# Kernel optimization log

Measured on AMD Instinct MI355X. Metric: run time of the kernel, lower is better.

## Reference

```python
import jax, jax.numpy as jnp
import numpy as np

B, T, IN, H = 1024, 200, 128, 128

def _linear_params(key, out_dim, in_dim):
    kw, kb = jax.random.split(key)
    bound = 1.0 / np.sqrt(in_dim)
    w = jax.random.uniform(kw, (out_dim, in_dim), jnp.float32, -bound, bound)
    b = jax.random.uniform(kb, (out_dim,), jnp.float32, -bound, bound)
    return w, b

def setup_inputs() -> dict:
    key = jax.random.key(0)
    ks = jax.random.split(key, 10)
    targets = jax.random.normal(ks[0], (B, T, IN), jnp.float32)
    history_states = jax.random.normal(ks[1], (B, T, H), jnp.float32)
    W_w, W_b = _linear_params(ks[2], H, IN)
    xu_w, xu_b = _linear_params(ks[3], H, H)
    hu_w, hu_b = _linear_params(ks[4], H, H)
    xr_w, xr_b = _linear_params(ks[5], H, H)
    hr_w, hr_b = _linear_params(ks[6], H, H)
    xg_w, xg_b = _linear_params(ks[7], H, H)
    hg_w, hg_b = _linear_params(ks[8], H, H)
    ln2_w, ln2_b = _linear_params(ks[9], H, IN + H)
    return dict(targets=targets, history_states=history_states,
                W_w=W_w, W_b=W_b, xu_w=xu_w, xu_b=xu_b, hu_w=hu_w, hu_b=hu_b,
                xr_w=xr_w, xr_b=xr_b, hr_w=hr_w, hr_b=hr_b,
                xg_w=xg_w, xg_b=xg_b, hg_w=hg_w, hg_b=hg_b,
                ln2_w=ln2_w, ln2_b=ln2_b)

def reference(targets, history_states, W_w, W_b, xu_w, xu_b, hu_w, hu_b,
              xr_w, xr_b, hr_w, hr_b, xg_w, xg_b, hg_w, hg_b, ln2_w, ln2_b):
    # attention weights: softmax over time of <W(targets), history>
    aw = jnp.einsum('bti,hi->bth', targets, W_w) + W_b            # [B,T,H]
    att = jax.nn.softmax(jnp.sum(aw * history_states, -1, keepdims=True), axis=1)  # [B,T,1]

    # precompute input-side projections as big GEMMs (same math as per-step Linear)
    xu = jnp.einsum('bth,oh->bto', history_states, xu_w) + xu_b   # [B,T,H]
    xr = jnp.einsum('bth,oh->bto', history_states, xr_w) + xr_b
    xg = jnp.einsum('bth,oh->bto', history_states, xg_w) + xg_b

    def step(h, xs):
        xu_t, xr_t, xg_t, a_t = xs                                 # [B,H],[B,H],[B,H],[B,1]
        u = jax.nn.sigmoid(xu_t + h @ hu_w.T + hu_b) * a_t
        r = jax.nn.sigmoid(xr_t + h @ hr_w.T + hr_b)
        g = jnp.tanh(xg_t + r * (h @ hg_w.T + hg_b))
        h = (1.0 - u) * h + u * g
        return h, None

    h0 = jnp.zeros((targets.shape[0], hu_w.shape[0]), targets.dtype)
    # scan over time: move T to leading axis
    xs = (jnp.swapaxes(xu, 0, 1), jnp.swapaxes(xr, 0, 1),
          jnp.swapaxes(xg, 0, 1), jnp.swapaxes(att, 0, 1))
    h, _ = jax.lax.scan(step, h0, xs)

    out = jnp.concatenate([h, targets[:, 0]], axis=-1) @ ln2_w.T + ln2_b
    return out
```

## Files before the change

kernel.cpp:

```cpp
#include <hip/hip_runtime.h>

#define B_ 1024
#define T_ 200
#define H_ 128

typedef __attribute__((ext_vector_type(8))) short short8;
typedef __attribute__((ext_vector_type(4))) float f32x4;

#define MFMA(a, b, c) __builtin_amdgcn_mfma_f32_16x16x32_bf16((a), (b), (c), 0, 0, 0)

static __device__ __forceinline__ short f2bf(float f) {
  unsigned u = __float_as_uint(f);
  u += 0x7fffu + ((u >> 16) & 1u);
  return (short)(u >> 16);
}
static __device__ __forceinline__ float bf2f(short s) {
  return __uint_as_float(((unsigned)(unsigned short)s) << 16);
}
static __device__ __forceinline__ unsigned pack2bf_rne(float a, float b) {
  unsigned ua = __float_as_uint(a);
  ua += 0x7fffu + ((ua >> 16) & 1u);
  unsigned ub = __float_as_uint(b);
  ub += 0x7fffu + ((ub >> 16) & 1u);
  return (ua >> 16) | (ub & 0xFFFF0000u);
}
static __device__ __forceinline__ unsigned pack2bf_trunc(float a, float b) {
  return (__float_as_uint(a) >> 16) | (__float_as_uint(b) & 0xFFFF0000u);
}
static __device__ __forceinline__ float rcp_f(float x) { return __builtin_amdgcn_rcpf(x); }
static __device__ __forceinline__ void ck_barrier() {
  asm volatile("s_waitcnt lgkmcnt(0)\n\ts_barrier" ::: "memory");
}

__global__ __launch_bounds__(512, 1) void proj_scores_kernel(
    const float* __restrict__ tgt, const float* __restrict__ hist,
    const float* __restrict__ Ww, const float* __restrict__ Wb,
    float* __restrict__ scores, short* __restrict__ histbf) {
  const int tc = blockIdx.x, bb = blockIdx.y;
  const int nt = (tc == 12) ? 8 : 16;
  const int t0 = tc * 16;
  const int tid = threadIdx.x;
  const int lane = tid & 63, w = tid >> 6;
  const int n = lane & 15, q = lane >> 4;

  __shared__ short tgt_hi[2][16 * 128];
  __shared__ short tgt_lo[2][16 * 128];
  __shared__ float hist_f[2][16 * 132];
  __shared__ float sp[16 * 8];

  short8 whi[4], wlo[4];
  f32x4 wb4;
  {
    const int o = w * 16 + n;
#pragma unroll
    for (int ks = 0; ks < 4; ++ks) {
      const float* p = Ww + o * H_ + ks * 32 + q * 8;
      short8 h, l;
#pragma unroll
      for (int j = 0; j < 8; ++j) {
        float f = p[j];
        short hv = f2bf(f);
        h[j] = hv;
        l[j] = f2bf(f - bf2f(hv));
      }
      whi[ks] = h;
      wlo[ks] = l;
    }
    wb4 = *(const f32x4*)(Wb + w * 16 + q * 4);
  }

  const int sm = tid >> 5, cs = tid & 31;
  const int g = cs >> 1, half = cs & 1;
  const int spos16 = sm * 128 + ((g ^ (sm & 7)) * 8) + half * 4;
  const int sposf = sm * 132 + cs * 4;
  const size_t rowbase = ((size_t)(bb * 16 + sm) * T_) * H_ + cs * 4;

  const int cu = tid;
  const int cks = cu >> 7, crem = cu & 127, cwl = crem >> 1, chalf = crem & 1;
  const int crow = cwl & 15, ckb = cks * 32 + (cwl >> 4) * 8 + chalf * 4;

  float4 hv = *(const float4*)(hist + rowbase + (size_t)t0 * H_);
  float4 tv = *(const float4*)(tgt + rowbase + (size_t)t0 * H_);
  {
    *(float4*)&hist_f[0][sposf] = hv;
    uint2 hi, lo;
    hi.x = pack2bf_rne(tv.x, tv.y);
    hi.y = pack2bf_rne(tv.z, tv.w);
    lo.x = pack2bf_rne(tv.x - bf2f((short)(hi.x)), tv.y - bf2f((short)(hi.x >> 16)));
    lo.y = pack2bf_rne(tv.z - bf2f((short)(hi.y)), tv.w - bf2f((short)(hi.y >> 16)));
    *(uint2*)&tgt_hi[0][spos16] = hi;
    *(uint2*)&tgt_lo[0][spos16] = lo;
  }
  ck_barrier();

  for (int tl = 0; tl < nt; ++tl) {
    const int cur = tl & 1, nxt = cur ^ 1;
    const bool have_next = (tl + 1 < nt);
    if (have_next) {
      hv = *(const float4*)(hist + rowbase + (size_t)(t0 + tl + 1) * H_);
      tv = *(const float4*)(tgt + rowbase + (size_t)(t0 + tl + 1) * H_);
    }
    f32x4 s1 = {0, 0, 0, 0}, s2 = {0, 0, 0, 0}, s3 = {0, 0, 0, 0};
#pragma unroll
    for (int ks = 0; ks < 4; ++ks) {
      const int fp = n * 128 + ((ks * 4 + q) ^ (n & 7)) * 8;
      short8 ahi = *(short8*)&tgt_hi[cur][fp];
      short8 alo = *(short8*)&tgt_lo[cur][fp];
      s1 = MFMA(whi[ks], ahi, s1);
      s2 = MFMA(wlo[ks], ahi, s2);
      s3 = MFMA(whi[ks], alo, s3);
    }
    {
      f32x4 hv4 = *(const f32x4*)&hist_f[cur][n * 132 + w * 16 + q * 4];
      float v = (s1[0] + s2[0] + s3[0] + wb4[0]) * hv4[0];
      v += (s1[1] + s2[1] + s3[1] + wb4[1]) * hv4[1];
      v += (s1[2] + s2[2] + s3[2] + wb4[2]) * hv4[2];
      v += (s1[3] + s2[3] + s3[3] + wb4[3]) * hv4[3];
      v += __shfl_xor(v, 16);
      v += __shfl_xor(v, 32);
      if (lane < 16) sp[n * 8 + w] = v;
    }
    if (histbf != nullptr) {
      const float* src = &hist_f[cur][crow * 132 + ckb];
      uint2 u;
      u.x = pack2bf_rne(src[0], src[1]);
      u.y = pack2bf_rne(src[2], src[3]);
      const size_t sb = (((size_t)(bb * T_ + t0 + tl) * 4) + cks) * 512 + cwl * 8 + chalf * 4;
      *(uint2*)(histbf + sb) = u;
    }
    if (have_next) {
      *(float4*)&hist_f[nxt][sposf] = hv;
      uint2 hi, lo;
      hi.x = pack2bf_rne(tv.x, tv.y);
      hi.y = pack2bf_rne(tv.z, tv.w);
      lo.x = pack2bf_rne(tv.x - bf2f((short)(hi.x)), tv.y - bf2f((short)(hi.x >> 16)));
      lo.y = pack2bf_rne(tv.z - bf2f((short)(hi.y)), tv.w - bf2f((short)(hi.y >> 16)));
      *(uint2*)&tgt_hi[nxt][spos16] = hi;
      *(uint2*)&tgt_lo[nxt][spos16] = lo;
    }
    ck_barrier();
    if (tid < 16) {
      float s = 0.0f;
#pragma unroll
      for (int ww = 0; ww < 8; ++ww) s += sp[tid * 8 + ww];
      scores[(size_t)(bb * 16 + tid) * T_ + (t0 + tl)] = s;
    }
    ck_barrier();
  }
}

__global__ __launch_bounds__(256, 4) void softmax_kernel(float* __restrict__ att) {
  const int b = blockIdx.x, tid = threadIdx.x;
  const int lane = tid & 63, wave = tid >> 6;
  __shared__ float red[8];
  float v = (tid < T_) ? att[(size_t)b * T_ + tid] : -3.0e38f;
  float mx = v;
#pragma unroll
  for (int d = 1; d < 64; d <<= 1) mx = fmaxf(mx, __shfl_xor(mx, d));
  if (lane == 0) red[wave] = mx;
  __syncthreads();
  mx = fmaxf(fmaxf(red[0], red[1]), fmaxf(red[2], red[3]));
  float e = (tid < T_) ? __expf(v - mx) : 0.0f;
  float sm = e;
#pragma unroll
  for (int d = 1; d < 64; d <<= 1) sm += __shfl_xor(sm, d);
  if (lane == 0) red[4 + wave] = sm;
  __syncthreads();
  sm = red[4] + red[5] + red[6] + red[7];
  if (tid < T_) att[(size_t)b * T_ + tid] = e / sm;
}

template <bool DIRECT>
__global__ __launch_bounds__(512, 1) void scan3_kernel(
    const float* __restrict__ hist,
    const float* __restrict__ xu_w, const float* __restrict__ xu_b,
    const float* __restrict__ hu_w, const float* __restrict__ hu_b,
    const float* __restrict__ xr_w, const float* __restrict__ xr_b,
    const float* __restrict__ hr_w, const float* __restrict__ hr_b,
    const float* __restrict__ xg_w, const float* __restrict__ xg_b,
    const float* __restrict__ hg_w, const float* __restrict__ hg_b,
    const float* __restrict__ att, const short* __restrict__ histbf,
    float* __restrict__ h_out) {
  const int tid = threadIdx.x;
  const int lane = tid & 63, w = tid >> 6;
  const int n = lane & 15, q = lane >> 4;
  const int bb = blockIdx.x, r0 = bb * 16;
  const int o = w * 16 + n;
  const int ob = w * 16 + q * 4;

  __shared__ short hbuf[2][16 * 128];
  __shared__ short xbuf[2][16 * 128];

  short8 wf[6][4];
  {
    const float* Wm[6] = {xu_w, hu_w, xr_w, hr_w, xg_w, hg_w};
#pragma unroll
    for (int M = 0; M < 6; ++M)
#pragma unroll
      for (int ks = 0; ks < 4; ++ks) {
        const float* p = Wm[M] + o * H_ + ks * 32 + q * 8;
        short8 v;
#pragma unroll
        for (int j = 0; j < 8; ++j) v[j] = f2bf(p[j]);
        wf[M][ks] = v;
      }
  }
  const f32x4 bu4 = *(const f32x4*)(xu_b + ob) + *(const f32x4*)(hu_b + ob);
  const f32x4 br4 = *(const f32x4*)(xr_b + ob) + *(const f32x4*)(hr_b + ob);
  const f32x4 bxg4 = *(const f32x4*)(xg_b + ob);
  const f32x4 bhg4 = *(const f32x4*)(hg_b + ob);

  for (int i = tid; i < 16 * 128; i += 512) hbuf[0][i] = 0;

  typedef union { uint4 u; short8 s; } frag_u;
  frag_u xp[2][4];
  const short* px = histbf + ((size_t)bb * T_ * 4) * 512 + (size_t)lane * 8;
  const int sm = tid >> 5, cs = tid & 31;
  const int xpos = sm * 128 + (((cs >> 1) ^ (sm & 7)) * 8) + (cs & 1) * 4;
  const float* hrow = hist + ((size_t)(r0 + sm) * T_) * H_ + cs * 4;
  float4 xnext;

  f32x4 xq[2][3];

  if constexpr (DIRECT) {
    frag_u x0[4];
#pragma unroll
    for (int ks = 0; ks < 4; ++ks)
      x0[ks].u = *(const uint4*)(px + (size_t)(0 * 4 + ks) * 512);
#pragma unroll
    for (int ks = 0; ks < 4; ++ks)
      xp[1][ks].u = *(const uint4*)(px + (size_t)(1 * 4 + ks) * 512);
#pragma unroll
    for (int ks = 0; ks < 4; ++ks)
      xp[0][ks].u = *(const uint4*)(px + (size_t)(2 * 4 + ks) * 512);
    xq[0][0] = bu4;
    xq[0][1] = br4;
    xq[0][2] = bxg4;
#pragma unroll
    for (int ks = 0; ks < 4; ++ks) {
      xq[0][0] = MFMA(wf[0][ks], x0[ks].s, xq[0][0]);
      xq[0][1] = MFMA(wf[2][ks], x0[ks].s, xq[0][1]);
      xq[0][2] = MFMA(wf[4][ks], x0[ks].s, xq[0][2]);
    }
  } else {
    float4 a = *(const float4*)hrow;
    uint2 u;
    u.x = pack2bf_rne(a.x, a.y);
    u.y = pack2bf_rne(a.z, a.w);
    *(uint2*)&xbuf[0][xpos] = u;
    xnext = *(const float4*)(hrow + H_);
  }

  float ap2[2];
  const float* pa = att + (size_t)(r0 + n) * T_;
  ap2[0] = pa[0];
  ap2[1] = pa[1];

  float hreg[4] = {0.0f, 0.0f, 0.0f, 0.0f};
  const int wri = n * 128 + (((w * 2 + (q >> 1)) ^ (n & 7)) * 8) + (q & 1) * 4;
  ck_barrier();

#pragma unroll 2
  for (int t = 0; t < T_; ++t) {
    const int cur = t & 1, nxt = cur ^ 1;
    short8 ha[4];
#pragma unroll
    for (int ks = 0; ks < 4; ++ks)
      ha[ks] = *(short8*)&hbuf[cur][n * 128 + ((ks * 4 + q) ^ (n & 7)) * 8];

    f32x4 ahu = {0, 0, 0, 0}, ahr = {0, 0, 0, 0}, ahg = bhg4;
#pragma unroll
    for (int ks = 0; ks < 4; ++ks) {
      ahu = MFMA(wf[1][ks], ha[ks], ahu);
      ahr = MFMA(wf[3][ks], ha[ks], ahr);
      ahg = MFMA(wf[5][ks], ha[ks], ahg);
    }

    if constexpr (!DIRECT) {
      short8 xa[4];
#pragma unroll
      for (int ks = 0; ks < 4; ++ks)
        xa[ks] = *(short8*)&xbuf[cur][n * 128 + ((ks * 4 + q) ^ (n & 7)) * 8];
      xq[cur][0] = bu4;
      xq[cur][1] = br4;
      xq[cur][2] = bxg4;
#pragma unroll
      for (int ks = 0; ks < 4; ++ks) {
        xq[cur][0] = MFMA(wf[0][ks], xa[ks], xq[cur][0]);
        xq[cur][1] = MFMA(wf[2][ks], xa[ks], xq[cur][1]);
        xq[cur][2] = MFMA(wf[4][ks], xa[ks], xq[cur][2]);
      }
    }

    const int tp = (t + 2 < T_) ? t + 2 : T_ - 1;
    const float at = ap2[cur];
    ap2[cur] = pa[tp];

    float hn[4];
#pragma unroll
    for (int r = 0; r < 4; ++r) {
      const float su = xq[cur][0][r] + ahu[r];
      const float uu = at * rcp_f(1.0f + __expf(-su));
      const float sr = xq[cur][1][r] + ahr[r];
      const float rr = rcp_f(1.0f + __expf(-sr));
      const float sg = xq[cur][2][r] + rr * ahg[r];
      const float g = 2.0f * rcp_f(1.0f + __expf(-2.0f * sg)) - 1.0f;
      hn[r] = hreg[r] + uu * (g - hreg[r]);
      hreg[r] = hn[r];
      if constexpr (DIRECT) {
        const short8 xs = xp[nxt][r].s;
        xq[nxt][0] = MFMA(wf[0][r], xs, (r == 0) ? bu4 : xq[nxt][0]);
        xq[nxt][1] = MFMA(wf[2][r], xs, (r == 0) ? br4 : xq[nxt][1]);
        xq[nxt][2] = MFMA(wf[4][r], xs, (r == 0) ? bxg4 : xq[nxt][2]);
      }
    }

    uint2 up;
    up.x = pack2bf_trunc(hn[0], hn[1]);
    up.y = pack2bf_trunc(hn[2], hn[3]);
    *(uint2*)&hbuf[nxt][wri] = up;

    if constexpr (DIRECT) {
      const int tf = (t + 3 < T_) ? t + 3 : T_ - 1;
#pragma unroll
      for (int ks = 0; ks < 4; ++ks)
        xp[nxt][ks].u = *(const uint4*)(px + (size_t)(tf * 4 + ks) * 512);
    } else {
      uint2 u;
      u.x = pack2bf_rne(xnext.x, xnext.y);
      u.y = pack2bf_rne(xnext.z, xnext.w);
      *(uint2*)&xbuf[nxt][xpos] = u;
      xnext = *(const float4*)(hrow + (size_t)tp * H_);
    }
    ck_barrier();
  }

  f32x4 hv = {hreg[0], hreg[1], hreg[2], hreg[3]};
  *(f32x4*)(h_out + (size_t)(r0 + n) * H_ + ob) = hv;
}

__global__ __launch_bounds__(256, 4) void final_kernel(
    const float* __restrict__ tgt, const float* __restrict__ hfin,
    const float* __restrict__ w, const float* __restrict__ bias,
    float* __restrict__ out) {
  const int b = blockIdx.x, tid = threadIdx.x;
  const int o = tid >> 1, half = tid & 1;
  const float* src = half ? (tgt + (size_t)b * (T_ * H_)) : (hfin + (size_t)b * H_);
  const float* wrow = w + o * 256 + half * 128;
  float acc = 0.0f;
#pragma unroll 8
  for (int k = 0; k < 128; k += 4) {
    float4 sv = *(const float4*)(src + k);
    float4 wv = *(const float4*)(wrow + k);
    acc += sv.x * wv.x + sv.y * wv.y + sv.z * wv.z + sv.w * wv.w;
  }
  acc += __shfl_xor(acc, 1);
  if (half == 0) out[(size_t)b * H_ + o] = acc + bias[o];
}

extern "C" void kernel_launch(void* const* d_in, const int* in_sizes, int n_in,
                              void* d_out, int out_size, void* d_ws, size_t ws_size,
                              hipStream_t stream) {
  const float* targets = (const float*)d_in[0];
  const float* history = (const float*)d_in[1];
  const float* W_w = (const float*)d_in[2];
  const float* W_b = (const float*)d_in[3];
  const float* xu_w = (const float*)d_in[4];
  const float* xu_b = (const float*)d_in[5];
  const float* hu_w = (const float*)d_in[6];
  const float* hu_b = (const float*)d_in[7];
  const float* xr_w = (const float*)d_in[8];
  const float* xr_b = (const float*)d_in[9];
  const float* hr_w = (const float*)d_in[10];
  const float* hr_b = (const float*)d_in[11];
  const float* xg_w = (const float*)d_in[12];
  const float* xg_b = (const float*)d_in[13];
  const float* hg_w = (const float*)d_in[14];
  const float* hg_b = (const float*)d_in[15];
  const float* ln2_w = (const float*)d_in[16];
  const float* ln2_b = (const float*)d_in[17];
  float* out = (float*)d_out;

  float* att = (float*)d_ws;
  float* hfin = att + (size_t)B_ * T_;
  const size_t fixed = (size_t)B_ * T_ * 4 + (size_t)B_ * H_ * 4;
  const size_t histbf_bytes = (size_t)64 * T_ * 4 * 512 * 8 * 2;
  short* histbf = (ws_size >= fixed + histbf_bytes)
                      ? (short*)((char*)d_ws + fixed)
                      : nullptr;

  proj_scores_kernel<<<dim3(13, 64), dim3(512), 0, stream>>>(
      targets, history, W_w, W_b, att, histbf);
  softmax_kernel<<<dim3(B_), dim3(256), 0, stream>>>(att);
  if (histbf) {
    scan3_kernel<true><<<dim3(64), dim3(512), 0, stream>>>(
        history, xu_w, xu_b, hu_w, hu_b, xr_w, xr_b, hr_w, hr_b,
        xg_w, xg_b, hg_w, hg_b, att, histbf, hfin);
  } else {
    scan3_kernel<false><<<dim3(64), dim3(512), 0, stream>>>(
        history, xu_w, xu_b, hu_w, hu_b, xr_w, xr_b, hr_w, hr_b,
        xg_w, xg_b, hg_w, hg_b, att, histbf, hfin);
  }
  final_kernel<<<dim3(B_), dim3(256), 0, stream>>>(targets, hfin, ln2_w, ln2_b, out);
}
```

Measured before the change: 464.9 us.

## Fold log2e scaling into GRU weights and pin step instruction schedule

Pre-scales the gate weight matrices and biases by log2(e), or 2*log2(e) for the candidate gate, so the sigmoid and tanh use the raw exp2 instruction with no multiply in front of it. This removes per-element multiplies from the serial recurrence step. It also adds sched_group_barrier directives in the DIRECT path to interleave LDS reads, MFMAs, global loads and VALU work in a fixed order. The result hinges on the hand-chosen group counts matching what the compiler emits. Folding the scale into the weights before bf16 rounding slightly changes numerics.

```diff
diff --git a/kernel.cpp b/kernel.cpp
--- a/kernel.cpp
+++ b/kernel.cpp
@@ -8,6 +8,13 @@
 typedef __attribute__((ext_vector_type(4))) float f32x4;
 
 #define MFMA(a, b, c) __builtin_amdgcn_mfma_f32_16x16x32_bf16((a), (b), (c), 0, 0, 0)
+
+#define SGB(mask, n) __builtin_amdgcn_sched_group_barrier((mask), (n), 0)
+#define SG_VALU 0x2
+#define SG_MFMA 0x8
+#define SG_VMEM_RD 0x20
+#define SG_DS_RD 0x100
+#define SG_DS_WR 0x200
 
 static __device__ __forceinline__ short f2bf(float f) {
   unsigned u = __float_as_uint(f);
@@ -28,6 +35,7 @@
   return (__float_as_uint(a) >> 16) | (__float_as_uint(b) & 0xFFFF0000u);
 }
 static __device__ __forceinline__ float rcp_f(float x) { return __builtin_amdgcn_rcpf(x); }
+static __device__ __forceinline__ float exp2_f(float x) { return __builtin_amdgcn_exp2f(x); }
 static __device__ __forceinline__ void ck_barrier() {
   asm volatile("s_waitcnt lgkmcnt(0)\n\ts_barrier" ::: "memory");
 }
@@ -188,12 +196,15 @@
   const int o = w * 16 + n;
   const int ob = w * 16 + q * 4;
 
+  constexpr float LOG2E = 1.4426950408889634f;
+
   __shared__ short hbuf[2][16 * 128];
   __shared__ short xbuf[2][16 * 128];
 
   short8 wf[6][4];
   {
     const float* Wm[6] = {xu_w, hu_w, xr_w, hr_w, xg_w, hg_w};
+    const float Sc[6] = {LOG2E, LOG2E, LOG2E, LOG2E, 2.0f * LOG2E, 2.0f * LOG2E};
 #pragma unroll
     for (int M = 0; M < 6; ++M)
 #pragma unroll
@@ -201,14 +212,14 @@
         const float* p = Wm[M] + o * H_ + ks * 32 + q * 8;
         short8 v;
 #pragma unroll
-        for (int j = 0; j < 8; ++j) v[j] = f2bf(p[j]);
+        for (int j = 0; j < 8; ++j) v[j] = f2bf(p[j] * Sc[M]);
         wf[M][ks] = v;
       }
   }
-  const f32x4 bu4 = *(const f32x4*)(xu_b + ob) + *(const f32x4*)(hu_b + ob);
-  const f32x4 br4 = *(const f32x4*)(xr_b + ob) + *(const f32x4*)(hr_b + ob);
-  const f32x4 bxg4 = *(const f32x4*)(xg_b + ob);
-  const f32x4 bhg4 = *(const f32x4*)(hg_b + ob);
+  const f32x4 bu4 = (*(const f32x4*)(xu_b + ob) + *(const f32x4*)(hu_b + ob)) * LOG2E;
+  const f32x4 br4 = (*(const f32x4*)(xr_b + ob) + *(const f32x4*)(hr_b + ob)) * LOG2E;
+  const f32x4 bxg4 = *(const f32x4*)(xg_b + ob) * (2.0f * LOG2E);
+  const f32x4 bhg4 = *(const f32x4*)(hg_b + ob) * (2.0f * LOG2E);
 
   for (int i = tid; i < 16 * 128; i += 512) hbuf[0][i] = 0;
 
@@ -300,11 +311,11 @@
 #pragma unroll
     for (int r = 0; r < 4; ++r) {
       const float su = xq[cur][0][r] + ahu[r];
-      const float uu = at * rcp_f(1.0f + __expf(-su));
+      const float uu = at * rcp_f(1.0f + exp2_f(-su));
       const float sr = xq[cur][1][r] + ahr[r];
-      const float rr = rcp_f(1.0f + __expf(-sr));
+      const float rr = rcp_f(1.0f + exp2_f(-sr));
       const float sg = xq[cur][2][r] + rr * ahg[r];
-      const float g = 2.0f * rcp_f(1.0f + __expf(-2.0f * sg)) - 1.0f;
+      const float g = 2.0f * rcp_f(1.0f + exp2_f(-sg)) - 1.0f;
       hn[r] = hreg[r] + uu * (g - hreg[r]);
       hreg[r] = hn[r];
       if constexpr (DIRECT) {
@@ -325,6 +336,19 @@
 #pragma unroll
       for (int ks = 0; ks < 4; ++ks)
         xp[nxt][ks].u = *(const uint4*)(px + (size_t)(tf * 4 + ks) * 512);
+      SGB(SG_DS_RD, 4);
+      SGB(SG_MFMA, 12);
+      SGB(SG_VMEM_RD, 5);
+      SGB(SG_VALU, 16);
+      SGB(SG_MFMA, 3);
+      SGB(SG_VALU, 16);
+      SGB(SG_MFMA, 3);
+      SGB(SG_VALU, 16);
+      SGB(SG_MFMA, 3);
+      SGB(SG_VALU, 16);
+      SGB(SG_MFMA, 3);
+      SGB(SG_VALU, 8);
+      SGB(SG_DS_WR, 1);
     } else {
       uint2 u;
       u.x = pack2bf_rne(xnext.x, xnext.y);
```

After: 450.1 us. -3.2%, faster.

## Restructure GRU scan: prescale weights by log2e, chain x/h MFMAs, unroll by 8

Applied to the files above, without the earlier changes.

The scan kernel now folds log2(e) and 2·log2(e) into the bf16 weights and biases, so the gates use exp2 directly with no per-element multiply. The x-projection result is used as the MFMA accumulator seed for the h-projection, which removes separate adds. The direct path is unrolled by 8, and attention weights are loaded as float4 vectors. The projection kernel double-buffers the score partials and drops one barrier per tile, and the bf16 history buffer gets a padded time stride (T+4) so the prefetch can read past the end safely. Pre-scaling before bf16 rounding slightly changes numerics, and the larger unroll may raise register pressure.

```diff
diff --git a/kernel.cpp b/kernel.cpp
--- a/kernel.cpp
+++ b/kernel.cpp
@@ -3,6 +3,7 @@
 #define B_ 1024
 #define T_ 200
 #define H_ 128
+#define TSTR (T_ + 4)
 
 typedef __attribute__((ext_vector_type(8))) short short8;
 typedef __attribute__((ext_vector_type(4))) float f32x4;
@@ -28,6 +29,7 @@
   return (__float_as_uint(a) >> 16) | (__float_as_uint(b) & 0xFFFF0000u);
 }
 static __device__ __forceinline__ float rcp_f(float x) { return __builtin_amdgcn_rcpf(x); }
+static __device__ __forceinline__ float exp2_f(float x) { return __builtin_amdgcn_exp2f(x); }
 static __device__ __forceinline__ void ck_barrier() {
   asm volatile("s_waitcnt lgkmcnt(0)\n\ts_barrier" ::: "memory");
 }
@@ -46,7 +48,7 @@
   __shared__ short tgt_hi[2][16 * 128];
   __shared__ short tgt_lo[2][16 * 128];
   __shared__ float hist_f[2][16 * 132];
-  __shared__ float sp[16 * 8];
+  __shared__ float sp[2][16 * 8];
 
   short8 whi[4], wlo[4];
   f32x4 wb4;
@@ -118,14 +120,15 @@
       v += (s1[3] + s2[3] + s3[3] + wb4[3]) * hv4[3];
       v += __shfl_xor(v, 16);
       v += __shfl_xor(v, 32);
-      if (lane < 16) sp[n * 8 + w] = v;
+      if (lane < 16) sp[cur][n * 8 + w] = v;
     }
     if (histbf != nullptr) {
       const float* src = &hist_f[cur][crow * 132 + ckb];
       uint2 u;
       u.x = pack2bf_rne(src[0], src[1]);
       u.y = pack2bf_rne(src[2], src[3]);
-      const size_t sb = (((size_t)(bb * T_ + t0 + tl) * 4) + cks) * 512 + cwl * 8 + chalf * 4;
+      const size_t sb =
+          (((size_t)(bb * TSTR + t0 + tl) * 4) + cks) * 512 + cwl * 8 + chalf * 4;
       *(uint2*)(histbf + sb) = u;
     }
     if (have_next) {
@@ -142,10 +145,9 @@
     if (tid < 16) {
       float s = 0.0f;
 #pragma unroll
-      for (int ww = 0; ww < 8; ++ww) s += sp[tid * 8 + ww];
+      for (int ww = 0; ww < 8; ++ww) s += sp[cur][tid * 8 + ww];
       scores[(size_t)(bb * 16 + tid) * T_ + (t0 + tl)] = s;
     }
-    ck_barrier();
   }
 }
 
@@ -188,12 +190,15 @@
   const int o = w * 16 + n;
   const int ob = w * 16 + q * 4;
 
+  constexpr float LOG2E = 1.4426950408889634f;
+
   __shared__ short hbuf[2][16 * 128];
   __shared__ short xbuf[2][16 * 128];
 
   short8 wf[6][4];
   {
     const float* Wm[6] = {xu_w, hu_w, xr_w, hr_w, xg_w, hg_w};
+    const float Sc[6] = {LOG2E, LOG2E, LOG2E, LOG2E, 2.0f * LOG2E, 2.0f * LOG2E};
 #pragma unroll
     for (int M = 0; M < 6; ++M)
 #pragma unroll
@@ -201,20 +206,20 @@
         const float* p = Wm[M] + o * H_ + ks * 32 + q * 8;
         short8 v;
 #pragma unroll
-        for (int j = 0; j < 8; ++j) v[j] = f2bf(p[j]);
+        for (int j = 0; j < 8; ++j) v[j] = f2bf(p[j] * Sc[M]);
         wf[M][ks] = v;
       }
   }
-  const f32x4 bu4 = *(const f32x4*)(xu_b + ob) + *(const f32x4*)(hu_b + ob);
-  const f32x4 br4 = *(const f32x4*)(xr_b + ob) + *(const f32x4*)(hr_b + ob);
-  const f32x4 bxg4 = *(const f32x4*)(xg_b + ob);
-  const f32x4 bhg4 = *(const f32x4*)(hg_b + ob);
+  const f32x4 bu4 = (*(const f32x4*)(xu_b + ob) + *(const f32x4*)(hu_b + ob)) * LOG2E;
+  const f32x4 br4 = (*(const f32x4*)(xr_b + ob) + *(const f32x4*)(hr_b + ob)) * LOG2E;
+  const f32x4 bxg4 = *(const f32x4*)(xg_b + ob) * (2.0f * LOG2E);
+  const f32x4 bhg4 = *(const f32x4*)(hg_b + ob) * (2.0f * LOG2E);
 
   for (int i = tid; i < 16 * 128; i += 512) hbuf[0][i] = 0;
 
   typedef union { uint4 u; short8 s; } frag_u;
   frag_u xp[2][4];
-  const short* px = histbf + ((size_t)bb * T_ * 4) * 512 + (size_t)lane * 8;
+  const short* px = histbf + ((size_t)bb * TSTR * 4) * 512 + (size_t)lane * 8;
   const int sm = tid >> 5, cs = tid & 31;
   const int xpos = sm * 128 + (((cs >> 1) ^ (sm & 7)) * 8) + (cs & 1) * 4;
   const float* hrow = hist + ((size_t)(r0 + sm) * T_) * H_ + cs * 4;
@@ -233,11 +238,11 @@
 #pragma unroll
     for (int ks = 0; ks < 4; ++ks)
       xp[0][ks].u = *(const uint4*)(px + (size_t)(2 * 4 + ks) * 512);
-    xq[0][0] = bu4;
-    xq[0][1] = br4;
-    xq[0][2] = bxg4;
-#pragma unroll
-    for (int ks = 0; ks < 4; ++ks) {
+    xq[0][0] = MFMA(wf[0][0], x0[0].s, bu4);
+    xq[0][1] = MFMA(wf[2][0], x0[0].s, br4);
+    xq[0][2] = MFMA(wf[4][0], x0[0].s, bxg4);
+#pragma unroll
+    for (int ks = 1; ks < 4; ++ks) {
       xq[0][0] = MFMA(wf[0][ks], x0[ks].s, xq[0][0]);
       xq[0][1] = MFMA(wf[2][ks], x0[ks].s, xq[0][1]);
       xq[0][2] = MFMA(wf[4][ks], x0[ks].s, xq[0][2]);
@@ -251,88 +256,131 @@
     xnext = *(const float4*)(hrow + H_);
   }
 
-  float ap2[2];
   const float* pa = att + (size_t)(r0 + n) * T_;
-  ap2[0] = pa[0];
-  ap2[1] = pa[1];
+  f32x4 ab0 = *(const f32x4*)(pa + 0);
+  f32x4 ab1 = *(const f32x4*)(pa + 4);
 
   float hreg[4] = {0.0f, 0.0f, 0.0f, 0.0f};
   const int wri = n * 128 + (((w * 2 + (q >> 1)) ^ (n & 7)) * 8) + (q & 1) * 4;
   ck_barrier();
 
+  if constexpr (DIRECT) {
+    const short* pxt = px + (size_t)12 * 512;
+    for (int tb = 0; tb < T_; tb += 8) {
+#pragma unroll
+      for (int k = 0; k < 8; ++k) {
+        const int t = tb + k;
+        const int cur = k & 1, nxt = cur ^ 1;
+        short8 ha[4];
+#pragma unroll
+        for (int ks = 0; ks < 4; ++ks)
+          ha[ks] = *(short8*)&hbuf[cur][n * 128 + ((ks * 4 + q) ^ (n & 7)) * 8];
+
+        f32x4 ahu = MFMA(wf[1][0], ha[0], xq[cur][0]);
+        f32x4 ahr = MFMA(wf[3][0], ha[0], xq[cur][1]);
+        f32x4 ahg = MFMA(wf[5][0], ha[0], bhg4);
+#pragma unroll
+        for (int ks = 1; ks < 4; ++ks) {
+          ahu = MFMA(wf[1][ks], ha[ks], ahu);
+          ahr = MFMA(wf[3][ks], ha[ks], ahr);
+          ahg = MFMA(wf[5][ks], ha[ks], ahg);
+        }
+
+        {
+          const short8 x0s = xp[nxt][0].s;
+          xq[nxt][0] = MFMA(wf[0][0], x0s, bu4);
+          xq[nxt][1] = MFMA(wf[2][0], x0s, br4);
+          xq[nxt][2] = MFMA(wf[4][0], x0s, bxg4);
+#pragma unroll
+          for (int ks = 1; ks < 4; ++ks) {
+            const short8 xs = xp[nxt][ks].s;
+            xq[nxt][0] = MFMA(wf[0][ks], xs, xq[nxt][0]);
+            xq[nxt][1] = MFMA(wf[2][ks], xs, xq[nxt][1]);
+            xq[nxt][2] = MFMA(wf[4][ks], xs, xq[nxt][2]);
+          }
+        }
+#pragma unroll
+        for (int ks = 0; ks < 4; ++ks)
+          xp[nxt][ks].u = *(const uint4*)(pxt + (size_t)(k * 4 + ks) * 512);
+
+        const float at = ((k >> 2) & 1) ? ab1[k & 3] : ab0[k & 3];
+        if (k == 3) ab0 = *(const f32x4*)(pa + ((t + 5 <= T_ - 4) ? t + 5 : T_ - 4));
+        if (k == 7) ab1 = *(const f32x4*)(pa + ((t + 5 <= T_ - 4) ? t + 5 : T_ - 4));
+
+        float hn[4];
+#pragma unroll
+        for (int r = 0; r < 4; ++r) {
+          const float uu = at * rcp_f(1.0f + exp2_f(-ahu[r]));
+          const float rr = rcp_f(1.0f + exp2_f(-ahr[r]));
+          const float sg = xq[cur][2][r] + rr * ahg[r];
+          const float g = 2.0f * rcp_f(1.0f + exp2_f(-sg)) - 1.0f;
+          hn[r] = hreg[r] + uu * (g - hreg[r]);
+          hreg[r] = hn[r];
+        }
+
+        uint2 up;
+        up.x = pack2bf_trunc(hn[0], hn[1]);
+        up.y = pack2bf_trunc(hn[2], hn[3]);
+        *(uint2*)&hbuf[nxt][wri] = up;
+        ck_barrier();
+      }
+      pxt += (size_t)8 * 4 * 512;
+    }
+  } else {
 #pragma unroll 2
-  for (int t = 0; t < T_; ++t) {
-    const int cur = t & 1, nxt = cur ^ 1;
-    short8 ha[4];
-#pragma unroll
-    for (int ks = 0; ks < 4; ++ks)
-      ha[ks] = *(short8*)&hbuf[cur][n * 128 + ((ks * 4 + q) ^ (n & 7)) * 8];
-
-    f32x4 ahu = {0, 0, 0, 0}, ahr = {0, 0, 0, 0}, ahg = bhg4;
-#pragma unroll
-    for (int ks = 0; ks < 4; ++ks) {
-      ahu = MFMA(wf[1][ks], ha[ks], ahu);
-      ahr = MFMA(wf[3][ks], ha[ks], ahr);
-      ahg = MFMA(wf[5][ks], ha[ks], ahg);
-    }
-
-    if constexpr (!DIRECT) {
+    for (int t = 0; t < T_; ++t) {
+      const int cur = t & 1, nxt = cur ^ 1;
+      short8 ha[4];
+#pragma unroll
+      for (int ks = 0; ks < 4; ++ks)
+        ha[ks] = *(short8*)&hbuf[cur][n * 128 + ((ks * 4 + q) ^ (n & 7)) * 8];
       short8 xa[4];
 #pragma unroll
       for (int ks = 0; ks < 4; ++ks)
         xa[ks] = *(short8*)&xbuf[cur][n * 128 + ((ks * 4 + q) ^ (n & 7)) * 8];
-      xq[cur][0] = bu4;
-      xq[cur][1] = br4;
-      xq[cur][2] = bxg4;
-#pragma unroll
-      for (int ks = 0; ks < 4; ++ks) {
-        xq[cur][0] = MFMA(wf[0][ks], xa[ks], xq[cur][0]);
-        xq[cur][1] = MFMA(wf[2][ks], xa[ks], xq[cur][1]);
-        xq[cur][2] = MFMA(wf[4][ks], xa[ks], xq[cur][2]);
-      }
-    }
-
-    const int tp = (t + 2 < T_) ? t + 2 : T_ - 1;
-    const float at = ap2[cur];
-    ap2[cur] = pa[tp];
-
-    float hn[4];
-#pragma unroll
-    for (int r = 0; r < 4; ++r) {
-      const float su = xq[cur][0][r] + ahu[r];
-      const float uu = at * rcp_f(1.0f + __expf(-su));
-      const float sr = xq[cur][1][r] + ahr[r];
-      const float rr = rcp_f(1.0f + __expf(-sr));
-      const float sg = xq[cur][2][r] + rr * ahg[r];
-      const float g = 2.0f * rcp_f(1.0f + __expf(-2.0f * sg)) - 1.0f;
-      hn[r] = hreg[r] + uu * (g - hreg[r]);
-      hreg[r] = hn[r];
-      if constexpr (DIRECT) {
-        const short8 xs = xp[nxt][r].s;
-        xq[nxt][0] = MFMA(wf[0][r], xs, (r == 0) ? bu4 : xq[nxt][0]);
-        xq[nxt][1] = MFMA(wf[2][r], xs, (r == 0) ? br4 : xq[nxt][1]);
-        xq[nxt][2] = MFMA(wf[4][r], xs, (r == 0) ? bxg4 : xq[nxt][2]);
-      }
-    }
-
-    uint2 up;
-    up.x = pack2bf_trunc(hn[0], hn[1]);
-    up.y = pack2bf_trunc(hn[2], hn[3]);
-    *(uint2*)&hbuf[nxt][wri] = up;
-
-    if constexpr (DIRECT) {
-      const int tf = (t + 3 < T_) ? t + 3 : T_ - 1;
-#pragma unroll
-      for (int ks = 0; ks < 4; ++ks)
-        xp[nxt][ks].u = *(const uint4*)(px + (size_t)(tf * 4 + ks) * 512);
-    } else {
+      f32x4 xu_a = MFMA(wf[0][0], xa[0], bu4);
+      f32x4 xr_a = MFMA(wf[2][0], xa[0], br4);
+      f32x4 xg_a = MFMA(wf[4][0], xa[0], bxg4);
+#pragma unroll
+      for (int ks = 1; ks < 4; ++ks) {
+        xu_a = MFMA(wf[0][ks], xa[ks], xu_a);
+        xr_a = MFMA(wf[2][ks], xa[ks], xr_a);
+        xg_a = MFMA(wf[4][ks], xa[ks], xg_a);
+      }
+      f32x4 ahu = MFMA(wf[1][0], ha[0], xu_a);
+      f32x4 ahr = MFMA(wf[3][0], ha[0], xr_a);
+      f32x4 ahg = MFMA(wf[5][0], ha[0], bhg4);
+#pragma unroll
+      for (int ks = 1; ks < 4; ++ks) {
+        ahu = MFMA(wf[1][ks], ha[ks], ahu);
+        ahr = MFMA(wf[3][ks], ha[ks], ahr);
+        ahg = MFMA(wf[5][ks], ha[ks], ahg);
+      }
+      const int tp = (t + 2 < T_) ? t + 2 : T_ - 1;
+      const float at = ((t >> 2) & 1) ? ab1[t & 3] : ab0[t & 3];
+      if ((t & 7) == 3) ab0 = *(const f32x4*)(pa + ((t + 5 <= T_ - 4) ? t + 5 : T_ - 4));
+      if ((t & 7) == 7) ab1 = *(const f32x4*)(pa + ((t + 5 <= T_ - 4) ? t + 5 : T_ - 4));
+      float hn[4];
+#pragma unroll
+      for (int r = 0; r < 4; ++r) {
+        const float uu = at * rcp_f(1.0f + exp2_f(-ahu[r]));
+        const float rr = rcp_f(1.0f + exp2_f(-ahr[r]));
+        const float sg = xg_a[r] + rr * ahg[r];
+        const float g = 2.0f * rcp_f(1.0f + exp2_f(-sg)) - 1.0f;
+        hn[r] = hreg[r] + uu * (g - hreg[r]);
+        hreg[r] = hn[r];
+      }
+      uint2 up;
+      up.x = pack2bf_trunc(hn[0], hn[1]);
+      up.y = pack2bf_trunc(hn[2], hn[3]);
+      *(uint2*)&hbuf[nxt][wri] = up;
       uint2 u;
       u.x = pack2bf_rne(xnext.x, xnext.y);
       u.y = pack2bf_rne(xnext.z, xnext.w);
       *(uint2*)&xbuf[nxt][xpos] = u;
       xnext = *(const float4*)(hrow + (size_t)tp * H_);
-    }
-    ck_barrier();
+      ck_barrier();
+    }
   }
 
   f32x4 hv = {hreg[0], hreg[1], hreg[2], hreg[3]};
@@ -384,7 +432,7 @@
   float* att = (float*)d_ws;
   float* hfin = att + (size_t)B_ * T_;
   const size_t fixed = (size_t)B_ * T_ * 4 + (size_t)B_ * H_ * 4;
-  const size_t histbf_bytes = (size_t)64 * T_ * 4 * 512 * 8 * 2;
+  const size_t histbf_bytes = (size_t)64 * TSTR * 4 * 512 * 2;
   short* histbf = (ws_size >= fixed + histbf_bytes)
                       ? (short*)((char*)d_ws + fixed)
                       : nullptr;
```

After: 445.9 us. -4.1%, faster.
